# Optimization experiments

Measured on AMD Instinct MI355X. Metric: run time of the kernel, lower is better.

Reference implementation:

```python
import jax, jax.numpy as jnp
import numpy as np

B, S, D, H = 2, 2048, 1024, 16
DK = D // H


def setup_inputs() -> dict:
    key = jax.random.key(0)
    ks = jax.random.split(key, 12)
    scale = 1.0 / np.sqrt(D)
    inp = {
        "Q": jax.random.normal(ks[0], (B, S, D), jnp.float32),
        "K": jax.random.normal(ks[1], (B, S, D), jnp.float32),
        "V": jax.random.normal(ks[2], (B, S, D), jnp.float32),
        # causal mask, broadcastable to [B, H, S, S]; 0 -> masked
        "Mask": jnp.tril(jnp.ones((S, S), jnp.int32))[None, None],
        "Wq": jax.random.normal(ks[3], (D, D), jnp.float32) * scale,
        "bq": jnp.zeros((D,), jnp.float32),
        "Wk": jax.random.normal(ks[4], (D, D), jnp.float32) * scale,
        "bk": jnp.zeros((D,), jnp.float32),
        "Wv": jax.random.normal(ks[5], (D, D), jnp.float32) * scale,
        "bv": jnp.zeros((D,), jnp.float32),
        "Wo": jax.random.normal(ks[6], (D, D), jnp.float32) * scale,
        "bo": jnp.zeros((D,), jnp.float32),
    }
    return inp


def _heads(x):
    # [B, S, D] -> [B, H, S, DK]
    return x.reshape(B, S, H, DK).transpose(0, 2, 1, 3)


def reference(Q, K, V, Mask, Wq, bq, Wk, bk, Wv, bv, Wo, bo):
    q = _heads(Q @ Wq.T + bq)
    k = _heads(K @ Wk.T + bk)
    v = _heads(V @ Wv.T + bv)
    # NOTE: original module does NOT scale by 1/sqrt(d_k)
    logits = jnp.einsum("bhqd,bhkd->bhqk", q, k)
    logits = jnp.where(Mask == 0, jnp.float32(-1e9), logits)
    attn = jax.nn.softmax(logits, axis=-1)  # dropout p=0.0 -> identity
    ctx = jnp.einsum("bhqk,bhkd->bhqd", attn, v)
    ctx = ctx.transpose(0, 2, 1, 3).reshape(B, S, D)
    return ctx @ Wo.T + bo
```

## Files before the change

kernel.cpp:

```cpp
#include <hip/hip_runtime.h>
#include <hip/hip_bf16.h>

#define B_  2
#define S_  2048
#define D_  1024
#define H_  16
#define DK_ 64
#define M_  (B_ * S_)

typedef __bf16 bf16;
typedef __bf16 bf16x8 __attribute__((ext_vector_type(8)));
typedef __bf16 bf16x4 __attribute__((ext_vector_type(4)));
typedef float  f32x4  __attribute__((ext_vector_type(4)));

#define MFMA16(a, b, c) __builtin_amdgcn_mfma_f32_16x16x32_bf16((a), (b), (c), 0, 0, 0)

__device__ __forceinline__ void gl2lds16(const bf16* g, bf16* l) {
    __builtin_amdgcn_global_load_lds((const __attribute__((address_space(1))) void*)g,
                                     (__attribute__((address_space(3))) void*)l, 16, 0, 0);
}

struct CastArgs { const float* src[7]; bf16* dst[7]; };

__global__ __launch_bounds__(256) void cast_all(CastArgs a) {
    int i = blockIdx.x * 256 + threadIdx.x;
    int seg, off;
    if (i < 3145728) { seg = i >> 20; off = i & 1048575; }
    else { int j = i - 3145728; seg = 3 + (j >> 18); off = j & 262143; }
    float4 v = ((const float4*)a.src[seg])[off];
    bf16x4 o;
    o[0] = (bf16)v.x; o[1] = (bf16)v.y; o[2] = (bf16)v.z; o[3] = (bf16)v.w;
    *(bf16x4*)&a.dst[seg][(size_t)off * 4] = o;
}

struct QkvArgs { const bf16* A[3]; const bf16* W[3]; const float* bias[3]; bf16* out[3]; };

__global__ __launch_bounds__(256, 3) void gemm_qkv(QkvArgs ar) {
    __shared__ char smem[34816];
    bf16* As = (bf16*)smem;
    bf16* Bs = (bf16*)(smem + 16384);
    bf16* Cs = (bf16*)smem;

    const int z = blockIdx.z;
    const bf16* A  = ar.A[z];
    const bf16* Bt = ar.W[z];
    const float* bias = ar.bias[z];
    bf16* Out = ar.out[z];
    const int mode = (z == 2) ? 1 : 0;

    const int t = threadIdx.x, lane = t & 63, w = t >> 6;
    const int lr = lane & 15, lq = lane >> 4;
    const int wm = (w >> 1) * 64, wn = (w & 1) * 64;
    const int n0 = blockIdx.x * 128, m0 = blockIdx.y * 128;

    const bf16* Ag[4]; const bf16* Bg[4]; bf16* Al[4]; bf16* Bl[4];
#pragma unroll
    for (int i = 0; i < 4; ++i) {
        int c = i * 256 + w * 64 + lane;
        int row = c >> 3, x = (c & 7) ^ (row & 7);
        Ag[i] = A  + (size_t)(m0 + row) * 1024 + x * 8;
        Bg[i] = Bt + (size_t)(n0 + row) * 1024 + x * 8;
        Al[i] = As + (i * 256 + w * 64) * 8;
        Bl[i] = Bs + (i * 256 + w * 64) * 8;
    }

    f32x4 acc[4][4];
#pragma unroll
    for (int mi = 0; mi < 4; ++mi)
#pragma unroll
        for (int ni = 0; ni < 4; ++ni) acc[mi][ni] = 0.0f;

    for (int k0 = 0; k0 < 1024; k0 += 64) {
        __syncthreads();
#pragma unroll
        for (int i = 0; i < 4; ++i) {
            gl2lds16(Ag[i] + k0, Al[i]);
            gl2lds16(Bg[i] + k0, Bl[i]);
        }
        __syncthreads();
#pragma unroll
        for (int ks = 0; ks < 2; ++ks) {
            bf16x8 af[4], bfr[4];
#pragma unroll
            for (int mi = 0; mi < 4; ++mi) {
                int row = wm + mi * 16 + lr;
                af[mi] = *(const bf16x8*)&As[row * 64 + ((ks * 4 + lq) ^ (row & 7)) * 8];
            }
#pragma unroll
            for (int ni = 0; ni < 4; ++ni) {
                int row = wn + ni * 16 + lr;
                bfr[ni] = *(const bf16x8*)&Bs[row * 64 + ((ks * 4 + lq) ^ (row & 7)) * 8];
            }
#pragma unroll
            for (int mi = 0; mi < 4; ++mi)
#pragma unroll
                for (int ni = 0; ni < 4; ++ni) acc[mi][ni] = MFMA16(af[mi], bfr[ni], acc[mi][ni]);
        }
    }

    if (mode == 0) {
#pragma unroll
        for (int mi = 0; mi < 4; ++mi) {
#pragma unroll
            for (int ni = 0; ni < 4; ++ni) {
                int gn = n0 + wn + ni * 16 + lr;
                float bv = bias[gn];
#pragma unroll
                for (int r = 0; r < 4; ++r) {
                    int gm = m0 + wm + mi * 16 + lq * 4 + r;
                    float v = acc[mi][ni][r] + bv;
                    int b = gm >> 11, s = gm & (S_ - 1);
                    int h = gn >> 6, dk = gn & 63;
                    Out[(((size_t)(b * H_ + h) * S_ + s) << 6) + dk] = (bf16)v;
                }
            }
        }
    } else {
        __syncthreads();
#pragma unroll
        for (int mi = 0; mi < 4; ++mi) {
#pragma unroll
            for (int ni = 0; ni < 4; ++ni) {
                int n = wn + ni * 16 + lr;
                float bv = bias[n0 + n];
                bf16x4 pk;
#pragma unroll
                for (int r = 0; r < 4; ++r) pk[r] = (bf16)(acc[mi][ni][r] + bv);
                *(bf16x4*)&Cs[n * 136 + wm + mi * 16 + lq * 4] = pk;
            }
        }
        __syncthreads();
        const int b = m0 >> 11, s0 = m0 & (S_ - 1);
#pragma unroll
        for (int j = 0; j < 8; ++j) {
            int cc = j * 256 + t;
            int n = cc >> 4, cm = cc & 15;
            int gn = n0 + n, h = gn >> 6, dk = gn & 63;
            bf16x8 v = *(const bf16x8*)&Cs[n * 136 + cm * 8];
            *(bf16x8*)&Out[(((size_t)(b * H_ + h) * DK_ + dk) << 11) + s0 + cm * 8] = v;
        }
    }
}

__global__ __launch_bounds__(256, 2) void gemm_out(const bf16* __restrict__ A,
                                                   const bf16* __restrict__ Bt,
                                                   const float* __restrict__ bias,
                                                   float* __restrict__ Out) {
    __shared__ bf16 As[64 * 64];
    __shared__ bf16 Bs[128 * 64];

    const int t = threadIdx.x, lane = t & 63, w = t >> 6;
    const int lr = lane & 15, lq = lane >> 4;
    const int wm = (w >> 1) * 32, wn = (w & 1) * 64;
    const int n0 = blockIdx.x * 128, m0 = blockIdx.y * 64;

    const bf16* Ag[2]; bf16* Al[2];
#pragma unroll
    for (int i = 0; i < 2; ++i) {
        int c = i * 256 + w * 64 + lane;
        int row = c >> 3, x = (c & 7) ^ (row & 7);
        Ag[i] = A + (size_t)(m0 + row) * 1024 + x * 8;
        Al[i] = As + (i * 256 + w * 64) * 8;
    }
    const bf16* Bg[4]; bf16* Bl[4];
#pragma unroll
    for (int i = 0; i < 4; ++i) {
        int c = i * 256 + w * 64 + lane;
        int row = c >> 3, x = (c & 7) ^ (row & 7);
        Bg[i] = Bt + (size_t)(n0 + row) * 1024 + x * 8;
        Bl[i] = Bs + (i * 256 + w * 64) * 8;
    }

    f32x4 acc[2][4];
#pragma unroll
    for (int mi = 0; mi < 2; ++mi)
#pragma unroll
        for (int ni = 0; ni < 4; ++ni) acc[mi][ni] = 0.0f;

    for (int k0 = 0; k0 < 1024; k0 += 64) {
        __syncthreads();
#pragma unroll
        for (int i = 0; i < 2; ++i) gl2lds16(Ag[i] + k0, Al[i]);
#pragma unroll
        for (int i = 0; i < 4; ++i) gl2lds16(Bg[i] + k0, Bl[i]);
        __syncthreads();
#pragma unroll
        for (int ks = 0; ks < 2; ++ks) {
            bf16x8 af[2], bfr[4];
#pragma unroll
            for (int mi = 0; mi < 2; ++mi) {
                int row = wm + mi * 16 + lr;
                af[mi] = *(const bf16x8*)&As[row * 64 + ((ks * 4 + lq) ^ (row & 7)) * 8];
            }
#pragma unroll
            for (int ni = 0; ni < 4; ++ni) {
                int row = wn + ni * 16 + lr;
                bfr[ni] = *(const bf16x8*)&Bs[row * 64 + ((ks * 4 + lq) ^ (row & 7)) * 8];
            }
#pragma unroll
            for (int mi = 0; mi < 2; ++mi)
#pragma unroll
                for (int ni = 0; ni < 4; ++ni) acc[mi][ni] = MFMA16(af[mi], bfr[ni], acc[mi][ni]);
        }
    }

#pragma unroll
    for (int mi = 0; mi < 2; ++mi) {
#pragma unroll
        for (int ni = 0; ni < 4; ++ni) {
            int gn = n0 + wn + ni * 16 + lr;
            float bv = bias[gn];
#pragma unroll
            for (int r = 0; r < 4; ++r) {
                int gm = m0 + wm + mi * 16 + lq * 4 + r;
                Out[(size_t)gm * 1024 + gn] = acc[mi][ni][r] + bv;
            }
        }
    }
}

__global__ __launch_bounds__(256, 3) void flash_attn(const bf16* __restrict__ qh,
                                                     const bf16* __restrict__ kh,
                                                     const bf16* __restrict__ vt,
                                                     bf16* __restrict__ ctx) {
    __shared__ char smem[49664];
    bf16* KsBuf[2];
    KsBuf[0] = (bf16*)smem;
    KsBuf[1] = (bf16*)(smem + 16384);
    bf16* Ps = (bf16*)(smem + 32768);
    float* Op = (float*)(smem + 32768);
    float* Lh = (float*)(smem + 49152);

    const int id = blockIdx.x;
    const int xcd = id & 7, loc = id >> 3;
    const int bh = xcd * 4 + (loc & 3);
    const int qt = 31 - (loc >> 2);
    const int b = bh >> 4, h = bh & 15;

    const bf16* Qp = qh + (size_t)bh * S_ * DK_;
    const bf16* Kp = kh + (size_t)bh * S_ * DK_;
    const bf16* Vp = vt + (size_t)bh * DK_ * S_;

    const int t = threadIdx.x, lane = t & 63, w = t >> 6;
    const int lr = lane & 15, lq = lane >> 4;
    const int wq = w & 1, wk = w >> 1;
    bf16* Pw = Ps + w * 2048;

    const bf16* Kg[4]; int Kloff[4];
#pragma unroll
    for (int i = 0; i < 4; ++i) {
        int c = w * 256 + i * 64 + lane;
        int krow = c >> 3, xx = (c & 7) ^ (krow & 7);
        Kg[i] = Kp + (size_t)krow * 64 + xx * 8;
        Kloff[i] = (w * 256 + i * 64) * 8;
    }

    bf16x8 qreg[2][2];
#pragma unroll
    for (int ks = 0; ks < 2; ++ks)
#pragma unroll
        for (int nt = 0; nt < 2; ++nt)
            qreg[ks][nt] = *(const bf16x8*)(Qp +
                (size_t)(qt * 64 + wq * 32 + nt * 16 + lr) * 64 + ks * 32 + lq * 8);

    f32x4 oacc[2][4];
#pragma unroll
    for (int mt = 0; mt < 2; ++mt)
#pragma unroll
        for (int nt = 0; nt < 4; ++nt) oacc[mt][nt] = 0.0f;
    float lpart[2] = {0.f, 0.f};

    const bf16* Vw = Vp + (size_t)lr * S_ + wk * 64 + lq * 8;

    const int nkt = qt / 2 + 1;

#pragma unroll
    for (int i = 0; i < 4; ++i) gl2lds16(Kg[i], KsBuf[0] + Kloff[i]);
    __syncthreads();

    for (int kt = 0; kt < nkt; ++kt) {
        bf16* Kc = KsBuf[kt & 1];
        if (kt + 1 < nkt) {
            bf16* Kn = KsBuf[(kt & 1) ^ 1];
#pragma unroll
            for (int i = 0; i < 4; ++i)
                gl2lds16(Kg[i] + (size_t)(kt + 1) * 8192, Kn + Kloff[i]);
        }

        const int k64 = kt * 2 + wk;
        if (k64 <= qt) {
            bf16x8 bv[2][4];
#pragma unroll
            for (int kk = 0; kk < 2; ++kk)
#pragma unroll
                for (int nt = 0; nt < 4; ++nt)
                    bv[kk][nt] = *(const bf16x8*)(Vw + (size_t)nt * 16 * S_ +
                                                  kt * 128 + kk * 32);
            f32x4 s[4][2];
#pragma unroll
            for (int mt = 0; mt < 4; ++mt)
#pragma unroll
                for (int nt = 0; nt < 2; ++nt) s[mt][nt] = 0.0f;
#pragma unroll
            for (int ks = 0; ks < 2; ++ks) {
                bf16x8 af[4];
                int xx = (ks * 4 + lq) ^ (lr & 7);
#pragma unroll
                for (int mt = 0; mt < 4; ++mt)
                    af[mt] = *(const bf16x8*)&Kc[(wk * 64 + mt * 16 + lr) * 64 + xx * 8];
#pragma unroll
                for (int mt = 0; mt < 4; ++mt)
#pragma unroll
                    for (int nt = 0; nt < 2; ++nt) s[mt][nt] = MFMA16(af[mt], qreg[ks][nt], s[mt][nt]);
            }
            const bool diag = (k64 == qt);
#pragma unroll
            for (int mt = 0; mt < 4; ++mt)
#pragma unroll
                for (int nt = 0; nt < 2; ++nt) {
                    bf16x4 pb;
#pragma unroll
                    for (int r = 0; r < 4; ++r) {
                        int kl = mt * 16 + lq * 4 + r;
                        int qlT = wq * 32 + nt * 16 + lr;
                        float p = (!diag || kl <= qlT) ? __expf(s[mt][nt][r]) : 0.0f;
                        bf16 p16 = (bf16)p;
                        lpart[nt] += (float)p16;
                        pb[r] = p16;
                    }
                    int xx = (2 * mt + (lq >> 1)) ^ (lr & 7);
                    *(bf16x4*)&Pw[(nt * 16 + lr) * 64 + xx * 8 + (lq & 1) * 4] = pb;
                }
#pragma unroll
            for (int kk = 0; kk < 2; ++kk) {
                bf16x8 ap[2];
                int xx = (kk * 4 + lq) ^ (lr & 7);
#pragma unroll
                for (int mt2 = 0; mt2 < 2; ++mt2)
                    ap[mt2] = *(const bf16x8*)&Pw[(mt2 * 16 + lr) * 64 + xx * 8];
#pragma unroll
                for (int mt2 = 0; mt2 < 2; ++mt2)
#pragma unroll
                    for (int nt = 0; nt < 4; ++nt)
                        oacc[mt2][nt] = MFMA16(ap[mt2], bv[kk][nt], oacc[mt2][nt]);
            }
        }
        __syncthreads();
    }

#pragma unroll
    for (int nt = 0; nt < 2; ++nt) {
        lpart[nt] += __shfl_xor(lpart[nt], 16);
        lpart[nt] += __shfl_xor(lpart[nt], 32);
    }
    if (lq == 0)
#pragma unroll
        for (int nt = 0; nt < 2; ++nt) Lh[wk * 64 + wq * 32 + nt * 16 + lr] = lpart[nt];
    if (wk == 1) {
#pragma unroll
        for (int mt = 0; mt < 2; ++mt)
#pragma unroll
            for (int nt = 0; nt < 4; ++nt)
#pragma unroll
                for (int r = 0; r < 4; ++r) {
                    int row = mt * 16 + lq * 4 + r, col = nt * 16 + lr;
                    int xx = (col >> 2) ^ (row & 15);
                    Op[wq * 2048 + row * 64 + xx * 4 + (col & 3)] = oacc[mt][nt][r];
                }
    }
    __syncthreads();
    if (wk == 0) {
        float linv[2][4];
#pragma unroll
        for (int mt = 0; mt < 2; ++mt)
#pragma unroll
            for (int r = 0; r < 4; ++r) {
                int qq = wq * 32 + mt * 16 + lq * 4 + r;
                linv[mt][r] = 1.0f / (Lh[qq] + Lh[64 + qq]);
            }
#pragma unroll
        for (int mt = 0; mt < 2; ++mt)
#pragma unroll
            for (int nt = 0; nt < 4; ++nt)
#pragma unroll
                for (int r = 0; r < 4; ++r) {
                    int row = mt * 16 + lq * 4 + r, col = nt * 16 + lr;
                    int xx = (col >> 2) ^ (row & 15);
                    float v = (oacc[mt][nt][r] + Op[wq * 2048 + row * 64 + xx * 4 + (col & 3)]) * linv[mt][r];
                    int q = qt * 64 + wq * 32 + row;
                    ctx[((size_t)(b * S_ + q)) * D_ + h * DK_ + col] = (bf16)v;
                }
    }
}

extern "C" void kernel_launch(void* const* d_in, const int* in_sizes, int n_in,
                              void* d_out, int out_size, void* d_ws, size_t ws_size,
                              hipStream_t stream) {
    const float* Q  = (const float*)d_in[0];
    const float* K  = (const float*)d_in[1];
    const float* V  = (const float*)d_in[2];
    const float* Wq = (const float*)d_in[4];
    const float* bq = (const float*)d_in[5];
    const float* Wk = (const float*)d_in[6];
    const float* bk = (const float*)d_in[7];
    const float* Wv = (const float*)d_in[8];
    const float* bv = (const float*)d_in[9];
    const float* Wo = (const float*)d_in[10];
    const float* bo = (const float*)d_in[11];

    char* p = (char*)d_ws;
    bf16* Qb  = (bf16*)p;  p += (size_t)M_ * D_ * 2;
    bf16* Kb  = (bf16*)p;  p += (size_t)M_ * D_ * 2;
    bf16* Vb  = (bf16*)p;  p += (size_t)M_ * D_ * 2;
    bf16* Wqb = (bf16*)p;  p += (size_t)D_ * D_ * 2;
    bf16* Wkb = (bf16*)p;  p += (size_t)D_ * D_ * 2;
    bf16* Wvb = (bf16*)p;  p += (size_t)D_ * D_ * 2;
    bf16* Wob = (bf16*)p;  p += (size_t)D_ * D_ * 2;
    bf16* qhd = (bf16*)p;  p += (size_t)M_ * D_ * 2;
    bf16* khd = (bf16*)p;  p += (size_t)M_ * D_ * 2;
    bf16* vtr = (bf16*)p;  p += (size_t)M_ * D_ * 2;
    bf16* ctx = (bf16*)p;  p += (size_t)M_ * D_ * 2;

    CastArgs ca;
    ca.src[0] = Q;  ca.dst[0] = Qb;
    ca.src[1] = K;  ca.dst[1] = Kb;
    ca.src[2] = V;  ca.dst[2] = Vb;
    ca.src[3] = Wq; ca.dst[3] = Wqb;
    ca.src[4] = Wk; ca.dst[4] = Wkb;
    ca.src[5] = Wv; ca.dst[5] = Wvb;
    ca.src[6] = Wo; ca.dst[6] = Wob;
    cast_all<<<16384, 256, 0, stream>>>(ca);

    QkvArgs qa;
    qa.A[0] = Qb;  qa.A[1] = Kb;  qa.A[2] = Vb;
    qa.W[0] = Wqb; qa.W[1] = Wkb; qa.W[2] = Wvb;
    qa.bias[0] = bq; qa.bias[1] = bk; qa.bias[2] = bv;
    qa.out[0] = qhd; qa.out[1] = khd; qa.out[2] = vtr;
    dim3 qgrid(D_ / 128, M_ / 128, 3);
    gemm_qkv<<<qgrid, 256, 0, stream>>>(qa);

    flash_attn<<<1024, 256, 0, stream>>>(qhd, khd, vtr, ctx);

    dim3 ogrid(D_ / 128, M_ / 64);
    gemm_out<<<ogrid, 256, 0, stream>>>(ctx, Wob, bo, (float*)d_out);
}
```

Baseline: 240.7 us.

## Keep P in registers via transposed 16x16x16 MFMA, drop LDS staging for P

The PV product is now computed transposed (O^T = V^T P^T) with the 16x16x16 bf16 MFMA. The S-accumulator layout then matches the B-operand layout directly, so P never has to be written to and read back from LDS. Removing the P buffer shrinks shared memory from about 49KB to 32KB, which lets launch bounds rise to 4 blocks per CU, and the block-to-tile mapping is reshuffled to interleave q-tiles. The costs are twice as many smaller MFMAs, 8-byte V loads issued inside the inner loop, and possible register pressure at the higher occupancy.

```diff
diff --git a/kernel.cpp b/kernel.cpp
--- a/kernel.cpp
+++ b/kernel.cpp
@@ -12,8 +12,23 @@
 typedef __bf16 bf16x8 __attribute__((ext_vector_type(8)));
 typedef __bf16 bf16x4 __attribute__((ext_vector_type(4)));
 typedef float  f32x4  __attribute__((ext_vector_type(4)));
+typedef short  s16x4  __attribute__((ext_vector_type(4)));
 
 #define MFMA16(a, b, c) __builtin_amdgcn_mfma_f32_16x16x32_bf16((a), (b), (c), 0, 0, 0)
+
+static __device__ __forceinline__ f32x4 MFMAK16(s16x4 a, s16x4 b, f32x4 c) {
+#if __has_builtin(__builtin_amdgcn_mfma_f32_16x16x16bf16_1k)
+    return __builtin_amdgcn_mfma_f32_16x16x16bf16_1k(a, b, c, 0, 0, 0);
+#else
+    asm volatile("v_mfma_f32_16x16x16_bf16 %0, %1, %2, %0"
+                 : "+v"(c) : "v"(a), "v"(b));
+    return c;
+#endif
+}
+
+static __device__ __forceinline__ short bf2s(bf16 x) {
+    union { bf16 b; short s; } u; u.b = x; return u.s;
+}
 
 __device__ __forceinline__ void gl2lds16(const bf16* g, bf16* l) {
     __builtin_amdgcn_global_load_lds((const __attribute__((address_space(1))) void*)g,
@@ -219,22 +234,21 @@
     }
 }
 
-__global__ __launch_bounds__(256, 3) void flash_attn(const bf16* __restrict__ qh,
+__global__ __launch_bounds__(256, 4) void flash_attn(const bf16* __restrict__ qh,
                                                      const bf16* __restrict__ kh,
                                                      const bf16* __restrict__ vt,
                                                      bf16* __restrict__ ctx) {
-    __shared__ char smem[49664];
+    __shared__ char smem[32768];
     bf16* KsBuf[2];
     KsBuf[0] = (bf16*)smem;
     KsBuf[1] = (bf16*)(smem + 16384);
-    bf16* Ps = (bf16*)(smem + 32768);
-    float* Op = (float*)(smem + 32768);
-    float* Lh = (float*)(smem + 49152);
+    float* Op = (float*)smem;
+    float* Lh = (float*)(smem + 16384);
 
     const int id = blockIdx.x;
-    const int xcd = id & 7, loc = id >> 3;
-    const int bh = xcd * 4 + (loc & 3);
-    const int qt = 31 - (loc >> 2);
+    const int xcd = id & 7, u = id >> 3;
+    const int qt = ((u & 3) << 3) | ((u >> 2) & 7);
+    const int bh = xcd * 4 + (u >> 5);
     const int b = bh >> 4, h = bh & 15;
 
     const bf16* Qp = qh + (size_t)bh * S_ * DK_;
@@ -244,7 +258,6 @@
     const int t = threadIdx.x, lane = t & 63, w = t >> 6;
     const int lr = lane & 15, lq = lane >> 4;
     const int wq = w & 1, wk = w >> 1;
-    bf16* Pw = Ps + w * 2048;
 
     const bf16* Kg[4]; int Kloff[4];
 #pragma unroll
@@ -263,14 +276,14 @@
             qreg[ks][nt] = *(const bf16x8*)(Qp +
                 (size_t)(qt * 64 + wq * 32 + nt * 16 + lr) * 64 + ks * 32 + lq * 8);
 
-    f32x4 oacc[2][4];
-#pragma unroll
-    for (int mt = 0; mt < 2; ++mt)
-#pragma unroll
-        for (int nt = 0; nt < 4; ++nt) oacc[mt][nt] = 0.0f;
+    f32x4 oaccT[4][2];
+#pragma unroll
+    for (int dkt = 0; dkt < 4; ++dkt)
+#pragma unroll
+        for (int nt = 0; nt < 2; ++nt) oaccT[dkt][nt] = 0.0f;
     float lpart[2] = {0.f, 0.f};
 
-    const bf16* Vw = Vp + (size_t)lr * S_ + wk * 64 + lq * 8;
+    const bf16* VwA = Vp + (size_t)lr * S_ + wk * 64 + lq * 4;
 
     const int nkt = qt / 2 + 1;
 
@@ -289,13 +302,6 @@
 
         const int k64 = kt * 2 + wk;
         if (k64 <= qt) {
-            bf16x8 bv[2][4];
-#pragma unroll
-            for (int kk = 0; kk < 2; ++kk)
-#pragma unroll
-                for (int nt = 0; nt < 4; ++nt)
-                    bv[kk][nt] = *(const bf16x8*)(Vw + (size_t)nt * 16 * S_ +
-                                                  kt * 128 + kk * 32);
             f32x4 s[4][2];
 #pragma unroll
             for (int mt = 0; mt < 4; ++mt)
@@ -315,10 +321,16 @@
             }
             const bool diag = (k64 == qt);
 #pragma unroll
-            for (int mt = 0; mt < 4; ++mt)
+            for (int mt = 0; mt < 4; ++mt) {
+                s16x4 vfrag[4];
+#pragma unroll
+                for (int dkt = 0; dkt < 4; ++dkt)
+                    vfrag[dkt] = *(const s16x4*)(VwA + (size_t)dkt * 16 * S_ +
+                                                 kt * 128 + mt * 16);
+                s16x4 pfrag[2];
 #pragma unroll
                 for (int nt = 0; nt < 2; ++nt) {
-                    bf16x4 pb;
+                    s16x4 pf;
 #pragma unroll
                     for (int r = 0; r < 4; ++r) {
                         int kl = mt * 16 + lq * 4 + r;
@@ -326,23 +338,15 @@
                         float p = (!diag || kl <= qlT) ? __expf(s[mt][nt][r]) : 0.0f;
                         bf16 p16 = (bf16)p;
                         lpart[nt] += (float)p16;
-                        pb[r] = p16;
+                        pf[r] = bf2s(p16);
                     }
-                    int xx = (2 * mt + (lq >> 1)) ^ (lr & 7);
-                    *(bf16x4*)&Pw[(nt * 16 + lr) * 64 + xx * 8 + (lq & 1) * 4] = pb;
+                    pfrag[nt] = pf;
                 }
 #pragma unroll
-            for (int kk = 0; kk < 2; ++kk) {
-                bf16x8 ap[2];
-                int xx = (kk * 4 + lq) ^ (lr & 7);
-#pragma unroll
-                for (int mt2 = 0; mt2 < 2; ++mt2)
-                    ap[mt2] = *(const bf16x8*)&Pw[(mt2 * 16 + lr) * 64 + xx * 8];
-#pragma unroll
-                for (int mt2 = 0; mt2 < 2; ++mt2)
-#pragma unroll
-                    for (int nt = 0; nt < 4; ++nt)
-                        oacc[mt2][nt] = MFMA16(ap[mt2], bv[kk][nt], oacc[mt2][nt]);
+                for (int dkt = 0; dkt < 4; ++dkt)
+#pragma unroll
+                    for (int nt = 0; nt < 2; ++nt)
+                        oaccT[dkt][nt] = MFMAK16(vfrag[dkt], pfrag[nt], oaccT[dkt][nt]);
             }
         }
         __syncthreads();
@@ -358,38 +362,34 @@
         for (int nt = 0; nt < 2; ++nt) Lh[wk * 64 + wq * 32 + nt * 16 + lr] = lpart[nt];
     if (wk == 1) {
 #pragma unroll
-        for (int mt = 0; mt < 2; ++mt)
-#pragma unroll
-            for (int nt = 0; nt < 4; ++nt)
-#pragma unroll
-                for (int r = 0; r < 4; ++r) {
-                    int row = mt * 16 + lq * 4 + r, col = nt * 16 + lr;
-                    int xx = (col >> 2) ^ (row & 15);
-                    Op[wq * 2048 + row * 64 + xx * 4 + (col & 3)] = oacc[mt][nt][r];
-                }
+        for (int dkt = 0; dkt < 4; ++dkt)
+#pragma unroll
+            for (int nt = 0; nt < 2; ++nt) {
+                int q32 = nt * 16 + lr, c = dkt * 4 + lq;
+                *(f32x4*)&Op[wq * 2048 + q32 * 64 + ((c ^ (q32 & 15)) << 2)] = oaccT[dkt][nt];
+            }
     }
     __syncthreads();
     if (wk == 0) {
-        float linv[2][4];
-#pragma unroll
-        for (int mt = 0; mt < 2; ++mt)
-#pragma unroll
-            for (int r = 0; r < 4; ++r) {
-                int qq = wq * 32 + mt * 16 + lq * 4 + r;
-                linv[mt][r] = 1.0f / (Lh[qq] + Lh[64 + qq]);
-            }
-#pragma unroll
-        for (int mt = 0; mt < 2; ++mt)
-#pragma unroll
-            for (int nt = 0; nt < 4; ++nt)
-#pragma unroll
-                for (int r = 0; r < 4; ++r) {
-                    int row = mt * 16 + lq * 4 + r, col = nt * 16 + lr;
-                    int xx = (col >> 2) ^ (row & 15);
-                    float v = (oacc[mt][nt][r] + Op[wq * 2048 + row * 64 + xx * 4 + (col & 3)]) * linv[mt][r];
-                    int q = qt * 64 + wq * 32 + row;
-                    ctx[((size_t)(b * S_ + q)) * D_ + h * DK_ + col] = (bf16)v;
-                }
+        float linv[2];
+#pragma unroll
+        for (int nt = 0; nt < 2; ++nt) {
+            int qq = wq * 32 + nt * 16 + lr;
+            linv[nt] = 1.0f / (Lh[qq] + Lh[64 + qq]);
+        }
+#pragma unroll
+        for (int dkt = 0; dkt < 4; ++dkt)
+#pragma unroll
+            for (int nt = 0; nt < 2; ++nt) {
+                int q32 = nt * 16 + lr, c = dkt * 4 + lq;
+                f32x4 o2 = *(const f32x4*)&Op[wq * 2048 + q32 * 64 + ((c ^ (q32 & 15)) << 2)];
+                bf16x4 ov;
+#pragma unroll
+                for (int r = 0; r < 4; ++r)
+                    ov[r] = (bf16)((oaccT[dkt][nt][r] + o2[r]) * linv[nt]);
+                int q = qt * 64 + wq * 32 + q32;
+                *(bf16x4*)&ctx[(size_t)(b * S_ + q) * D_ + h * DK_ + dkt * 16 + lq * 4] = ov;
+            }
     }
 }
 
```

After: 349.6 us. +45.2%, slower.
